# Performance work log

Hardware: AMD Instinct MI355X
Metric: run time of the kernel (lower is better)

Reference implementation:

```python
import jax, jax.numpy as jnp
import numpy as np

USER_NUM = 100000
ITEM_NUM = 100000
N_NODES = USER_NUM + ITEM_NUM
EMB = 64
N_EDGES = 6400000
N_LAYERS = 3
LAYER_CL = 1
EPS = 0.1


def setup_inputs() -> dict:
    key = jax.random.key(0)
    k1, k2, k3, k4, k5, k6 = jax.random.split(key, 6)
    # Xavier-uniform-like scale for embeddings
    scale = float(np.sqrt(6.0 / (USER_NUM + EMB)))
    user_emb = jax.random.normal(k1, (USER_NUM, EMB), dtype=jnp.float32) * scale
    item_emb = jax.random.normal(k2, (ITEM_NUM, EMB), dtype=jnp.float32) * scale
    adj_rows = jax.random.randint(k3, (N_EDGES,), 0, N_NODES, dtype=jnp.int64)
    adj_cols = jax.random.randint(k4, (N_EDGES,), 0, N_NODES, dtype=jnp.int64)
    # normalized adjacency values ~ 1/degree
    adj_vals = jax.random.uniform(k5, (N_EDGES,), dtype=jnp.float32) * (1.0 / 32.0)
    # precomputed uniform noise replacing torch.rand_like per layer
    noise = jax.random.uniform(k6, (N_LAYERS, N_NODES, EMB), dtype=jnp.float32)
    return {"user_emb": user_emb, "item_emb": item_emb, "adj_rows": adj_rows,
            "adj_cols": adj_cols, "adj_vals": adj_vals, "noise": noise}


def _spmm(rows, cols, vals, x):
    # sparse [N,N] @ dense [N,D] via gather + segment_sum
    return jax.ops.segment_sum(vals[:, None] * x[cols], rows, num_segments=N_NODES)


def reference(user_emb, item_emb, adj_rows, adj_cols, adj_vals, noise):
    ego = jnp.concatenate([user_emb, item_emb], axis=0)  # [N, D]
    cl = ego
    acc = jnp.zeros_like(ego)
    for k in range(N_LAYERS):
        ego = _spmm(adj_rows, adj_cols, adj_vals, ego)
        # perturbed branch: ego += sign(ego) * F.normalize(noise_k, dim=-1) * eps
        nk = noise[k]
        nrm = jnp.maximum(jnp.linalg.norm(nk, axis=-1, keepdims=True), 1e-12)
        ego = ego + jnp.sign(ego) * (nk / nrm) * EPS
        acc = acc + ego
        if k == LAYER_CL - 1:
            cl = ego
    final = acc / N_LAYERS  # mean over stacked layer outputs
    return (final[:USER_NUM], final[USER_NUM:], cl[:USER_NUM], cl[USER_NUM:])
```

## Files before the change

### kernel.cpp

```cpp
#include <hip/hip_runtime.h>


#define USER_NUM 100000
#define N_NODES  200000
#define EMB      64
#define N_EDGES  6400000
#define NBUCK    782
#define CAP      9216
#define EPB      16384
#define TB_A     1024
#define NBLK     391

static constexpr size_t BUFA_OFF  = 0;
static constexpr size_t BUFB_OFF  = 51200000;
static constexpr size_t CV_OFF    = 102400000;
static constexpr size_t RS_OFF    = 153600000;
static constexpr size_t SMALL_OFF = 154400016;
static constexpr size_t NRM_OFF   = 155200016;
static constexpr size_t WS_NEED   = 156000016;

__global__ __launch_bounds__(TB_A) void k_prep(const int* __restrict__ rows,
                                               const int* __restrict__ cols,
                                               const float* __restrict__ vals,
                                               int* __restrict__ bcnt_part,
                                               int2* __restrict__ zip) {
    __shared__ int h[NBUCK];
    for (int i = threadIdx.x; i < NBUCK; i += TB_A) h[i] = 0;
    __syncthreads();
    int base = blockIdx.x * EPB;
    int end  = min(base + EPB, N_EDGES);
    for (int e = base + threadIdx.x; e < end; e += TB_A) {
        atomicAdd(&h[rows[e] >> 8], 1);
        zip[e] = make_int2(cols[e], __float_as_int(vals[e]));
    }
    __syncthreads();
    for (int i = threadIdx.x; i < NBUCK; i += TB_A)
        bcnt_part[blockIdx.x * NBUCK + i] = h[i];
}

__global__ void k_scan782(const int* __restrict__ bcnt_part,
                          int* __restrict__ bcnt, int* __restrict__ bbase,
                          int* __restrict__ gcur, int* __restrict__ rs) {
    __shared__ int s[1024];
    int i = threadIdx.x;
    int v = 0;
    if (i < NBUCK) {
        for (int b = 0; b < NBLK; ++b) v += bcnt_part[b * NBUCK + i];
        bcnt[i] = v;
    }
    s[i] = v;
    __syncthreads();
    for (int off = 1; off < 1024; off <<= 1) {
        int t = 0;
        if (i >= off) t = s[i - off];
        __syncthreads();
        s[i] += t;
        __syncthreads();
    }
    if (i < NBUCK) {
        int ex = s[i] - v;
        bbase[i] = ex;
        gcur[i] = ex;
    }
    if (i == 0) rs[N_NODES] = N_EDGES;
}

__global__ __launch_bounds__(TB_A) void k_bin(const int* __restrict__ rows,
                                              int* __restrict__ gcur,
                                              int* __restrict__ keys) {
    __shared__ int h[NBUCK];
    __shared__ int gb[NBUCK];
    for (int i = threadIdx.x; i < NBUCK; i += TB_A) h[i] = 0;
    __syncthreads();
    int base = blockIdx.x * EPB;
    int end  = min(base + EPB, N_EDGES);
    for (int e = base + threadIdx.x; e < end; e += TB_A)
        atomicAdd(&h[rows[e] >> 8], 1);
    __syncthreads();
    for (int i = threadIdx.x; i < NBUCK; i += TB_A) {
        int c = h[i];
        gb[i] = c ? atomicAdd(&gcur[i], c) : 0;
        h[i] = 0;
    }
    __syncthreads();
    for (int e = base + threadIdx.x; e < end; e += TB_A) {
        int r = rows[e];
        int b = r >> 8;
        int pos = gb[b] + atomicAdd(&h[b], 1);
        keys[pos] = ((r & 255) << 24) | e;
    }
}

__global__ __launch_bounds__(256) void k_build(const int* __restrict__ keys,
                                               const int2* __restrict__ zip,
                                               const int* __restrict__ bcnt,
                                               const int* __restrict__ bbase,
                                               int2* __restrict__ cv,
                                               int* __restrict__ rs) {
    __shared__ int cnt[256];
    __shared__ int start[256];
    __shared__ int cur[256];
    __shared__ int scanbuf[256];
    __shared__ int eKey[CAP];
    int tid = threadIdx.x;
    int b = blockIdx.x;
    int n = bcnt[b];
    int base = bbase[b];
    int rowbase = b << 8;
    cnt[tid] = 0;
    __syncthreads();
    for (int i = tid; i < n; i += 256) {
        unsigned key = (unsigned)keys[base + i];
        atomicAdd(&cnt[key >> 24], 1);
    }
    __syncthreads();
    int v = cnt[tid];
    scanbuf[tid] = v;
    __syncthreads();
    for (int off = 1; off < 256; off <<= 1) {
        int t = 0;
        if (tid >= off) t = scanbuf[tid - off];
        __syncthreads();
        scanbuf[tid] += t;
        __syncthreads();
    }
    start[tid] = scanbuf[tid] - v;
    {
        int row = rowbase + tid;
        if (row < N_NODES) rs[row] = base + start[tid];
    }
    cur[tid] = 0;
    __syncthreads();
    if (n <= CAP) {
        for (int i = tid; i < n; i += 256) {
            int key = keys[base + i];
            int rl = (int)((unsigned)key >> 24);
            int p = start[rl] + atomicAdd(&cur[rl], 1);
            eKey[p] = key;
        }
        __syncthreads();
        for (int p = tid; p < n; p += 256) {
            int k = eKey[p];
            int rl = (int)((unsigned)k >> 24);
            int s0 = start[rl];
            int s1 = s0 + cnt[rl];
            int rank = 0;
            int q = s0;
            for (; q + 4 <= s1; q += 4) {
                rank += (eKey[q]     < k);
                rank += (eKey[q + 1] < k);
                rank += (eKey[q + 2] < k);
                rank += (eKey[q + 3] < k);
            }
            for (; q < s1; ++q) rank += (eKey[q] < k);
            int e = k & 0x00FFFFFF;
            cv[base + s0 + rank] = zip[e];
        }
    } else {
        for (int i = tid; i < n; i += 256) {
            int key = keys[base + i];
            int rl = (int)((unsigned)key >> 24);
            int p = start[rl] + atomicAdd(&cur[rl], 1);
            cv[base + p] = make_int2(key, 0);
        }
        __syncthreads();
        int c = cnt[tid];
        if (c > 1) {
            int s0 = start[tid];
            int s1 = s0 + c;
            for (int i = s0 + 1; i < s1; ++i) {
                int2 kv = cv[base + i];
                int j = i - 1;
                while (j >= s0 && cv[base + j].x > kv.x) {
                    cv[base + j + 1] = cv[base + j];
                    --j;
                }
                cv[base + j + 1] = kv;
            }
        }
        __syncthreads();
        for (int i = tid; i < n; i += 256) {
            int e = cv[base + i].x & 0x00FFFFFF;
            cv[base + i] = zip[e];
        }
    }
}

__global__ __launch_bounds__(256) void k_fused(const int* __restrict__ rs,
                                               const int2* __restrict__ cv,
                                               const float* __restrict__ xlo,
                                               const float* __restrict__ xhi,
                                               int split,
                                               const float* __restrict__ nk,
                                               float* __restrict__ ego,
                                               float* __restrict__ accF,
                                               float* __restrict__ clF,
                                               int mode) {
    int t = blockIdx.x * blockDim.x + threadIdx.x;
    int r = t >> 4;
    int u = t & 15;
    int c = u << 2;
    int idx = t << 2;
    float4 n4 = *(const float4*)(nk + idx);
    float q0 = __fmul_rn(n4.x, n4.x);
    float q1 = __fmul_rn(n4.y, n4.y);
    float q2 = __fmul_rn(n4.z, n4.z);
    float q3 = __fmul_rn(n4.w, n4.w);
    float f0 = q0, f1 = q1, f2 = q2, f3 = q3;
    #pragma unroll
    for (int s = 0; s < 7; ++s) {
        float g0 = __shfl_up(f0, 2, 16);
        float g1 = __shfl_up(f1, 2, 16);
        float g2 = __shfl_up(f2, 2, 16);
        float g3 = __shfl_up(f3, 2, 16);
        if (u >= 2) {
            f0 = __fadd_rn(g0, q0);
            f1 = __fadd_rn(g1, q1);
            f2 = __fadd_rn(g2, q2);
            f3 = __fadd_rn(g3, q3);
        }
    }
    float tAB = __fadd_rn(__fadd_rn(f0, f1), __fadd_rn(f2, f3));
    float tlo = __shfl(tAB, 14, 16);
    float thi = __shfl(tAB, 15, 16);
    float nv = __fsqrt_rn(__fadd_rn(tlo, thi));
    nv = fmaxf(nv, 1e-12f);
    int j0 = rs[r], j1 = rs[r + 1];
    float a0 = 0.f, a1 = 0.f, a2 = 0.f, a3 = 0.f;
    if (j0 < j1) {
        const int EMAX = N_EDGES - 1;
        #define XROW(col) (((col) < split ? xlo : xhi) + \
                           ((col) < split ? (col) : (col) - split) * EMB + c)
        int2 c0 = cv[j0];
        int2 c1 = cv[min(j0 + 1, EMAX)];
        int2 c2 = cv[min(j0 + 2, EMAX)];
        int2 n0 = cv[min(j0 + 3, EMAX)];
        int2 n1 = cv[min(j0 + 4, EMAX)];
        int2 n2 = cv[min(j0 + 5, EMAX)];
        int2 m0 = cv[min(j0 + 6, EMAX)];
        int2 m1 = cv[min(j0 + 7, EMAX)];
        int2 m2 = cv[min(j0 + 8, EMAX)];
        float4 x0 = *(const float4*)XROW(c0.x);
        float4 x1 = *(const float4*)XROW(c1.x);
        float4 x2 = *(const float4*)XROW(c2.x);
        for (int j = j0; j < j1; j += 3) {
            float4 y0 = *(const float4*)XROW(n0.x);
            float4 y1 = *(const float4*)XROW(n1.x);
            float4 y2 = *(const float4*)XROW(n2.x);
            float v0 = __int_as_float(c0.y);
            float v1 = (j + 1 < j1) ? __int_as_float(c1.y) : 0.f;
            float v2 = (j + 2 < j1) ? __int_as_float(c2.y) : 0.f;
            a0 = __fadd_rn(a0, __fmul_rn(v0, x0.x));
            a1 = __fadd_rn(a1, __fmul_rn(v0, x0.y));
            a2 = __fadd_rn(a2, __fmul_rn(v0, x0.z));
            a3 = __fadd_rn(a3, __fmul_rn(v0, x0.w));
            a0 = __fadd_rn(a0, __fmul_rn(v1, x1.x));
            a1 = __fadd_rn(a1, __fmul_rn(v1, x1.y));
            a2 = __fadd_rn(a2, __fmul_rn(v1, x1.z));
            a3 = __fadd_rn(a3, __fmul_rn(v1, x1.w));
            a0 = __fadd_rn(a0, __fmul_rn(v2, x2.x));
            a1 = __fadd_rn(a1, __fmul_rn(v2, x2.y));
            a2 = __fadd_rn(a2, __fmul_rn(v2, x2.z));
            a3 = __fadd_rn(a3, __fmul_rn(v2, x2.w));
            c0 = n0; c1 = n1; c2 = n2;
            n0 = m0; n1 = m1; n2 = m2;
            x0 = y0; x1 = y1; x2 = y2;
            m0 = cv[min(j + 9,  EMAX)];
            m1 = cv[min(j + 10, EMAX)];
            m2 = cv[min(j + 11, EMAX)];
        }
        #undef XROW
    }
    float4 e4;
    {
        float s, q;
        s = (a0 > 0.f) ? 1.f : ((a0 < 0.f) ? -1.f : 0.f);
        q = __fdiv_rn(n4.x, nv);
        e4.x = __fadd_rn(a0, __fmul_rn(__fmul_rn(s, q), 0.1f));
        s = (a1 > 0.f) ? 1.f : ((a1 < 0.f) ? -1.f : 0.f);
        q = __fdiv_rn(n4.y, nv);
        e4.y = __fadd_rn(a1, __fmul_rn(__fmul_rn(s, q), 0.1f));
        s = (a2 > 0.f) ? 1.f : ((a2 < 0.f) ? -1.f : 0.f);
        q = __fdiv_rn(n4.z, nv);
        e4.z = __fadd_rn(a2, __fmul_rn(__fmul_rn(s, q), 0.1f));
        s = (a3 > 0.f) ? 1.f : ((a3 < 0.f) ? -1.f : 0.f);
        q = __fdiv_rn(n4.w, nv);
        e4.w = __fadd_rn(a3, __fmul_rn(__fmul_rn(s, q), 0.1f));
    }
    if (mode == 0) {
        *(float4*)(ego + idx) = e4;
        *(float4*)(clF + idx) = e4;
    } else if (mode == 1) {
        *(float4*)(ego + idx) = e4;
        float4 a = *(const float4*)(clF + idx);
        a.x = __fadd_rn(a.x, e4.x);
        a.y = __fadd_rn(a.y, e4.y);
        a.z = __fadd_rn(a.z, e4.z);
        a.w = __fadd_rn(a.w, e4.w);
        *(float4*)(accF + idx) = a;
    } else {
        float4 a = *(const float4*)(accF + idx);
        float4 f;
        f.x = __fdiv_rn(__fadd_rn(a.x, e4.x), 3.0f);
        f.y = __fdiv_rn(__fadd_rn(a.y, e4.y), 3.0f);
        f.z = __fdiv_rn(__fadd_rn(a.z, e4.z), 3.0f);
        f.w = __fdiv_rn(__fadd_rn(a.w, e4.w), 3.0f);
        *(float4*)(accF + idx) = f;
    }
}

extern "C" void kernel_launch(void* const* d_in, const int* in_sizes, int n_in,
                              void* d_out, int out_size, void* d_ws, size_t ws_size,
                              hipStream_t stream) {
    if (ws_size < WS_NEED) return;

    const float* user_emb = (const float*)d_in[0];
    const float* item_emb = (const float*)d_in[1];
    const int*   adj_rows = (const int*)d_in[2];
    const int*   adj_cols = (const int*)d_in[3];
    const float* adj_vals = (const float*)d_in[4];
    const float* noise    = (const float*)d_in[5];

    char* ws = (char*)d_ws;
    float* bufA = (float*)(ws + BUFA_OFF);
    float* bufB = (float*)(ws + BUFB_OFF);
    int*   keys = (int*)(ws + BUFA_OFF);
    int2*  zip  = (int2*)(ws + BUFB_OFF);
    int*   bcnt_part = (int*)(ws + CV_OFF);
    int2*  cv   = (int2*)(ws + CV_OFF);
    int*   rs   = (int*)(ws + RS_OFF);
    int*   bcnt = (int*)(ws + SMALL_OFF);
    int*   bbase= (int*)(ws + SMALL_OFF + 3200);
    int*   gcur = (int*)(ws + SMALL_OFF + 6400);

    float* accF = (float*)d_out;
    float* clF  = (float*)d_out + (size_t)N_NODES * EMB;

    k_prep<<<NBLK, TB_A, 0, stream>>>(adj_rows, adj_cols, adj_vals, bcnt_part,
                                      zip);
    k_scan782<<<1, 1024, 0, stream>>>(bcnt_part, bcnt, bbase, gcur, rs);
    k_bin<<<NBLK, TB_A, 0, stream>>>(adj_rows, gcur, keys);
    k_build<<<NBUCK, 256, 0, stream>>>(keys, zip, bcnt, bbase, cv, rs);

    const int T16 = N_NODES * 16;
    for (int k = 0; k < 3; ++k) {
        const float* nkp = noise + (size_t)k * N_NODES * EMB;
        const float* xlo  = (k == 0) ? user_emb : ((k == 1) ? bufA : bufB);
        const float* xhi  = (k == 0) ? item_emb : ((k == 1) ? bufA : bufB);
        int split = (k == 0) ? USER_NUM : 0;
        float* ego_out = (k == 0) ? bufA : bufB;
        k_fused<<<T16 / 256, 256, 0, stream>>>(rs, cv, xlo, xhi, split,
                                               nkp, ego_out, accF, clF, k);
    }
}
```

Baseline: 1.232 ms.

## Reuse cl output as layer-1 input and use nontemporal streaming loads/stores

Layer 0 now writes only to the cl output and layer 1 gathers directly from it, which removes the duplicate ego buffer write. Layer 1 no longer writes an accumulator. The final layer rebuilds the sum from cl and the layer-1 buffer, so one full write and one full read of an N×64 array are gone. Streaming accesses (noise, the col/val list, and the outputs) now use nontemporal loads and stores to keep them from polluting the cache used by the gathered rows. The risk is that nontemporal hints on cv or clF could hurt if that data was benefiting from cache reuse.

Result: slower. 1.330 ms (+8.0%).

```diff
diff --git a/kernel.cpp b/kernel.cpp
--- a/kernel.cpp
+++ b/kernel.cpp
@@ -16,8 +16,23 @@
 static constexpr size_t CV_OFF    = 102400000;
 static constexpr size_t RS_OFF    = 153600000;
 static constexpr size_t SMALL_OFF = 154400016;
-static constexpr size_t NRM_OFF   = 155200016;
 static constexpr size_t WS_NEED   = 156000016;
+
+typedef float f4v __attribute__((ext_vector_type(4)));
+typedef int   i2v __attribute__((ext_vector_type(2)));
+
+__device__ __forceinline__ float4 ntload4(const float* p) {
+    f4v v = __builtin_nontemporal_load((const f4v*)p);
+    return make_float4(v.x, v.y, v.z, v.w);
+}
+__device__ __forceinline__ void ntstore4(float* p, float4 v) {
+    f4v t = {v.x, v.y, v.z, v.w};
+    __builtin_nontemporal_store(t, (f4v*)p);
+}
+__device__ __forceinline__ int2 ntload2(const int2* p) {
+    i2v v = __builtin_nontemporal_load((const i2v*)p);
+    return make_int2(v.x, v.y);
+}
 
 __global__ __launch_bounds__(TB_A) void k_prep(const int* __restrict__ rows,
                                                const int* __restrict__ cols,
@@ -201,7 +216,7 @@
     int u = t & 15;
     int c = u << 2;
     int idx = t << 2;
-    float4 n4 = *(const float4*)(nk + idx);
+    float4 n4 = ntload4(nk + idx);
     float q0 = __fmul_rn(n4.x, n4.x);
     float q1 = __fmul_rn(n4.y, n4.y);
     float q2 = __fmul_rn(n4.z, n4.z);
@@ -231,15 +246,15 @@
         const int EMAX = N_EDGES - 1;
         #define XROW(col) (((col) < split ? xlo : xhi) + \
                            ((col) < split ? (col) : (col) - split) * EMB + c)
-        int2 c0 = cv[j0];
-        int2 c1 = cv[min(j0 + 1, EMAX)];
-        int2 c2 = cv[min(j0 + 2, EMAX)];
-        int2 n0 = cv[min(j0 + 3, EMAX)];
-        int2 n1 = cv[min(j0 + 4, EMAX)];
-        int2 n2 = cv[min(j0 + 5, EMAX)];
-        int2 m0 = cv[min(j0 + 6, EMAX)];
-        int2 m1 = cv[min(j0 + 7, EMAX)];
-        int2 m2 = cv[min(j0 + 8, EMAX)];
+        int2 c0 = ntload2(&cv[j0]);
+        int2 c1 = ntload2(&cv[min(j0 + 1, EMAX)]);
+        int2 c2 = ntload2(&cv[min(j0 + 2, EMAX)]);
+        int2 n0 = ntload2(&cv[min(j0 + 3, EMAX)]);
+        int2 n1 = ntload2(&cv[min(j0 + 4, EMAX)]);
+        int2 n2 = ntload2(&cv[min(j0 + 5, EMAX)]);
+        int2 m0 = ntload2(&cv[min(j0 + 6, EMAX)]);
+        int2 m1 = ntload2(&cv[min(j0 + 7, EMAX)]);
+        int2 m2 = ntload2(&cv[min(j0 + 8, EMAX)]);
         float4 x0 = *(const float4*)XROW(c0.x);
         float4 x1 = *(const float4*)XROW(c1.x);
         float4 x2 = *(const float4*)XROW(c2.x);
@@ -265,9 +280,9 @@
             c0 = n0; c1 = n1; c2 = n2;
             n0 = m0; n1 = m1; n2 = m2;
             x0 = y0; x1 = y1; x2 = y2;
-            m0 = cv[min(j + 9,  EMAX)];
-            m1 = cv[min(j + 10, EMAX)];
-            m2 = cv[min(j + 11, EMAX)];
+            m0 = ntload2(&cv[min(j + 9,  EMAX)]);
+            m1 = ntload2(&cv[min(j + 10, EMAX)]);
+            m2 = ntload2(&cv[min(j + 11, EMAX)]);
         }
         #undef XROW
     }
@@ -288,24 +303,23 @@
         e4.w = __fadd_rn(a3, __fmul_rn(__fmul_rn(s, q), 0.1f));
     }
     if (mode == 0) {
-        *(float4*)(ego + idx) = e4;
-        *(float4*)(clF + idx) = e4;
+        ntstore4(clF + idx, e4);
     } else if (mode == 1) {
-        *(float4*)(ego + idx) = e4;
-        float4 a = *(const float4*)(clF + idx);
-        a.x = __fadd_rn(a.x, e4.x);
-        a.y = __fadd_rn(a.y, e4.y);
-        a.z = __fadd_rn(a.z, e4.z);
-        a.w = __fadd_rn(a.w, e4.w);
-        *(float4*)(accF + idx) = a;
+        ntstore4(ego + idx, e4);
     } else {
-        float4 a = *(const float4*)(accF + idx);
+        float4 cl4 = ntload4(clF + idx);
+        float4 x1 = *(const float4*)(xhi + idx);
+        float4 a;
+        a.x = __fadd_rn(cl4.x, x1.x);
+        a.y = __fadd_rn(cl4.y, x1.y);
+        a.z = __fadd_rn(cl4.z, x1.z);
+        a.w = __fadd_rn(cl4.w, x1.w);
         float4 f;
         f.x = __fdiv_rn(__fadd_rn(a.x, e4.x), 3.0f);
         f.y = __fdiv_rn(__fadd_rn(a.y, e4.y), 3.0f);
         f.z = __fdiv_rn(__fadd_rn(a.z, e4.z), 3.0f);
         f.w = __fdiv_rn(__fadd_rn(a.w, e4.w), 3.0f);
-        *(float4*)(accF + idx) = f;
+        ntstore4(accF + idx, f);
     }
 }
 
@@ -322,7 +336,6 @@
     const float* noise    = (const float*)d_in[5];
 
     char* ws = (char*)d_ws;
-    float* bufA = (float*)(ws + BUFA_OFF);
     float* bufB = (float*)(ws + BUFB_OFF);
     int*   keys = (int*)(ws + BUFA_OFF);
     int2*  zip  = (int2*)(ws + BUFB_OFF);
@@ -345,11 +358,10 @@
     const int T16 = N_NODES * 16;
     for (int k = 0; k < 3; ++k) {
         const float* nkp = noise + (size_t)k * N_NODES * EMB;
-        const float* xlo  = (k == 0) ? user_emb : ((k == 1) ? bufA : bufB);
-        const float* xhi  = (k == 0) ? item_emb : ((k == 1) ? bufA : bufB);
+        const float* xlo  = (k == 0) ? user_emb : ((k == 1) ? clF : bufB);
+        const float* xhi  = (k == 0) ? item_emb : ((k == 1) ? clF : bufB);
         int split = (k == 0) ? USER_NUM : 0;
-        float* ego_out = (k == 0) ? bufA : bufB;
         k_fused<<<T16 / 256, 256, 0, stream>>>(rs, cv, xlo, xhi, split,
-                                               nkp, ego_out, accF, clF, k);
-    }
-}
+                                               nkp, bufB, accF, clF, k);
+    }
+}
```
